# Optimization experiments

Measured on AMD Instinct MI355X. Metric: run time of the kernel, lower is better.

## Reference

```python
import jax, jax.numpy as jnp
import numpy as np

T, B, S, A, H = 512, 1024, 64, 16, 128  # timesteps, envs, state_dim, action_dim, LAYER_SIZE


def setup_inputs() -> dict:
    key = jax.random.key(0)
    ks = jax.random.split(key, 12)

    def w(k, shape, fan_in, std=1.0):
        return std * jax.random.normal(k, shape, jnp.float32) / jnp.sqrt(fan_in)

    x = jax.random.normal(ks[0], (T * B, S), jnp.float32)
    done = (jax.random.uniform(ks[1], (T * B,)) < 0.05).astype(jnp.float32)
    action = jax.random.randint(ks[2], (T * B,), 0, A, jnp.int32)
    gru_state = jnp.zeros((1, B, H), jnp.float32)

    return {
        "x": x, "done": done, "action": action, "gru_state": gru_state,
        "W1": w(ks[3], (H, S), S), "b1": jnp.zeros((H,), jnp.float32),
        "W2": w(ks[4], (H, H), H), "b2": jnp.zeros((H,), jnp.float32),
        "W_ih": w(ks[5], (3 * H, H), H), "b_ih": jnp.zeros((3 * H,), jnp.float32),
        "W_hh": w(ks[6], (3 * H, H), H), "b_hh": jnp.zeros((3 * H,), jnp.float32),
        "Wa": w(ks[7], (A, H), H, std=0.01), "ba": jnp.zeros((A,), jnp.float32),
        "Wc": w(ks[8], (1, H), H), "bc": jnp.zeros((1,), jnp.float32),
    }


def reference(x, done, action, gru_state, W1, b1, W2, b2, W_ih, b_ih, W_hh, b_hh, Wa, ba, Wc, bc):
    # MLP encoder: Linear->ReLU->Linear->ReLU  [T*B, H]
    h2 = jax.nn.relu(jax.nn.relu(x @ W1.T + b1) @ W2.T + b2)
    # Precompute input-side GRU gates for all timesteps: [T, B, 3H]
    gx = (h2 @ W_ih.T + b_ih).reshape(T, B, 3 * H)
    d = done.reshape(T, B)
    h0 = gru_state[0]  # [B, H]

    def step(h, inp):
        gx_t, d_t = inp
        h = (1.0 - d_t)[:, None] * h  # done-mask state reset
        gh = h @ W_hh.T + b_hh
        xr, xz, xn = jnp.split(gx_t, 3, axis=-1)
        hr, hz, hn = jnp.split(gh, 3, axis=-1)
        r = jax.nn.sigmoid(xr + hr)
        z = jax.nn.sigmoid(xz + hz)
        n = jnp.tanh(xn + r * hn)
        h_new = (1.0 - z) * n + z * h
        return h_new, h_new

    h_last, hs = jax.lax.scan(step, h0, (gx, d))
    hidden = hs.reshape(T * B, H)

    logits = hidden @ Wa.T + ba
    logp = jax.nn.log_softmax(logits, axis=-1)
    log_prob = jnp.take_along_axis(logp, action[:, None].astype(jnp.int32), axis=1)[:, 0]
    entropy = -jnp.sum(jnp.exp(logp) * logp, axis=-1)
    # DETACH=True: critic runs on detached hidden
    value = jax.lax.stop_gradient(hidden) @ Wc.T + bc  # [T*B, 1]

    main = jnp.concatenate([log_prob[:, None], entropy[:, None], value], axis=1)  # [T*B, 3]
    return main, h_last[None]
```

## Files before the change

kernel.cpp:

```cpp
#include <hip/hip_runtime.h>
#include <stdint.h>

#define TT 512
#define BB 1024
#define SS 64
#define HH 128
#define TBR (TT*BB)
#define NTILE (TBR/16)
#define MW_TPW 16
#define MGRID (NTILE/(4*MW_TPW))

typedef __attribute__((ext_vector_type(8))) short short8;
typedef __attribute__((ext_vector_type(4))) float floatx4;
typedef unsigned short u16;
typedef unsigned int u32;
typedef struct { u32 x, y; } u32x2;

struct TrueT  { static constexpr bool value = true;  };
struct FalseT { static constexpr bool value = false; };

__device__ __forceinline__ float bf2f(u16 u){union{u32 i;float f;}v;v.i=((u32)u)<<16;return v.f;}
__device__ __forceinline__ u16 f2bf(float f){union{float f;u32 i;}v;v.f=f;u32 r=v.i+0x7FFFu+((v.i>>16)&1u);return (u16)(r>>16);}
__device__ __forceinline__ float frcp(float x){ return __builtin_amdgcn_rcpf(x); }

__device__ __forceinline__ bool buf_is_bf16(const u16* p) {
  int ok = 0;
#pragma unroll
  for (int i = 0; i < 32; ++i) {
    u32 v = p[2*i] & 0x7FFFu;
    u32 e = v >> 7;
    ok += (v == 0u || (e >= 96u && e <= 128u)) ? 1 : 0;
  }
  return ok >= 24;
}

template<bool BF> __device__ __forceinline__ float ld1(const void* p, size_t i){
  if constexpr (BF) return bf2f(((const u16*)p)[i]);
  else              return ((const float*)p)[i];
}
__device__ __forceinline__ short8 pack8(floatx4 a, floatx4 b){
  short8 r;
  r[0]=(short)f2bf(a[0]); r[1]=(short)f2bf(a[1]); r[2]=(short)f2bf(a[2]); r[3]=(short)f2bf(a[3]);
  r[4]=(short)f2bf(b[0]); r[5]=(short)f2bf(b[1]); r[6]=(short)f2bf(b[2]); r[7]=(short)f2bf(b[3]);
  return r;
}
template<bool BF> __device__ __forceinline__ short8 ld8(const void* p, size_t i){
  if constexpr (BF) return *(const short8*)((const u16*)p + i);
  else {
    const float* f = (const float*)p + i;
    return pack8(*(const floatx4*)f, *(const floatx4*)(f + 4));
  }
}
template<bool BF> __device__ __forceinline__ void st1(void* p, size_t i, float v){
  if constexpr (BF) ((u16*)p)[i] = f2bf(v);
  else              ((float*)p)[i] = v;
}

__device__ __forceinline__ void barrier_lds() {
  __asm__ __volatile__("" ::: "memory");
  __builtin_amdgcn_s_waitcnt(0xC07F);
  __builtin_amdgcn_s_barrier();
  __asm__ __volatile__("" ::: "memory");
}

__device__ __forceinline__ int fragidx(int m,int k){
  return ((k>>5)<<9)+((m+(((k>>3)&3)<<4))<<3)+(k&7);
}
__device__ __forceinline__ floatx4 mfma(short8 a, short8 b, floatx4 c){
  return __builtin_amdgcn_mfma_f32_16x16x32_bf16(a,b,c,0,0,0);
}

template<bool BF>
__global__ __launch_bounds__(256, 2) void k_mlp(
    const void* __restrict__ x,
    const void* __restrict__ W1, const void* __restrict__ b1,
    const void* __restrict__ W2, const void* __restrict__ b2,
    u16* __restrict__ h2g)
{
  if (buf_is_bf16((const u16*)W1) != BF) return;
  const int tid = threadIdx.x, lane = tid & 63, wv = tid >> 6;
  const int n16 = lane & 15, q = lane >> 4;

  __shared__ __align__(16) u16 W2L[8*4*64*8];
  __shared__ __align__(16) u16 scr[4][2048];

  for (int s = tid; s < 2048; s += 256) {
    int j = s >> 8, ks = (s >> 6) & 3, l = s & 63;
    short8 v = ld8<BF>(W2, (size_t)(16*j + (l & 15))*HH + ks*32 + (l >> 4)*8);
    *(short8*)&W2L[(size_t)s*8] = v;
  }
  short8 w1b[8][2]; float b1v[8], b2v[8];
#pragma unroll
  for (int j = 0; j < 8; ++j) {
    int row = 16*j + n16;
#pragma unroll
    for (int ks = 0; ks < 2; ++ks) w1b[j][ks] = ld8<BF>(W1, (size_t)row*SS + ks*32 + q*8);
    b1v[j] = ld1<BF>(b1, row);
    b2v[j] = ld1<BF>(b2, row);
  }
  __syncthreads();

  u16* S = scr[wv];
  const int tile0 = (blockIdx.x * 4 + wv) * MW_TPW;

  short8 xb0, xb1; floatx4 xf0, xf1, xf2, xf3;
  {
    size_t base = ((size_t)tile0*16 + n16)*SS + q*8;
    if constexpr (BF) {
      xb0 = *(const short8*)((const u16*)x + base);
      xb1 = *(const short8*)((const u16*)x + base + 32);
    } else {
      const float* f = (const float*)x + base;
      xf0 = *(const floatx4*)f;       xf1 = *(const floatx4*)(f+4);
      xf2 = *(const floatx4*)(f+32);  xf3 = *(const floatx4*)(f+36);
    }
  }

  for (int i = 0; i < MW_TPW; ++i) {
    const int tau = tile0 + i;
    short8 xc0, xc1;
    if constexpr (BF) { xc0 = xb0; xc1 = xb1; }
    else              { xc0 = pack8(xf0, xf1); xc1 = pack8(xf2, xf3); }
    if (i + 1 < MW_TPW) {
      size_t base = ((size_t)(tau+1)*16 + n16)*SS + q*8;
      if constexpr (BF) {
        xb0 = *(const short8*)((const u16*)x + base);
        xb1 = *(const short8*)((const u16*)x + base + 32);
      } else {
        const float* f = (const float*)x + base;
        xf0 = *(const floatx4*)f;       xf1 = *(const floatx4*)(f+4);
        xf2 = *(const floatx4*)(f+32);  xf3 = *(const floatx4*)(f+36);
      }
    }
#pragma unroll
    for (int j = 0; j < 8; ++j) {
      floatx4 a = {0.f,0.f,0.f,0.f};
      a = mfma(xc0, w1b[j][0], a);
      a = mfma(xc1, w1b[j][1], a);
#pragma unroll
      for (int r = 0; r < 4; ++r) {
        float v = a[r] + b1v[j]; v = v > 0.f ? v : 0.f;
        S[fragidx(4*q + r, 16*j + n16)] = f2bf(v);
      }
    }
    short8 h1a0 = *(const short8*)(S + 0*512 + lane*8);
    short8 h1a1 = *(const short8*)(S + 1*512 + lane*8);
    short8 h1a2 = *(const short8*)(S + 2*512 + lane*8);
    short8 h1a3 = *(const short8*)(S + 3*512 + lane*8);
#pragma unroll
    for (int j = 0; j < 8; ++j) {
      floatx4 a = {0.f,0.f,0.f,0.f};
      a = mfma(h1a0, *(const short8*)&W2L[(size_t)((j*4+0)*64 + lane)*8], a);
      a = mfma(h1a1, *(const short8*)&W2L[(size_t)((j*4+1)*64 + lane)*8], a);
      a = mfma(h1a2, *(const short8*)&W2L[(size_t)((j*4+2)*64 + lane)*8], a);
      a = mfma(h1a3, *(const short8*)&W2L[(size_t)((j*4+3)*64 + lane)*8], a);
#pragma unroll
      for (int r = 0; r < 4; ++r) {
        float v = a[r] + b2v[j]; v = v > 0.f ? v : 0.f;
        S[fragidx(4*q + r, 16*j + n16)] = f2bf(v);
      }
    }
    {
      const u16* src = S + lane*32;
      u16* dst = h2g + (size_t)tau*2048 + lane*32;
      short8 d0 = *(const short8*)(src);
      short8 d1 = *(const short8*)(src + 8);
      short8 d2 = *(const short8*)(src + 16);
      short8 d3 = *(const short8*)(src + 24);
      *(short8*)(dst)      = d0;
      *(short8*)(dst + 8)  = d1;
      *(short8*)(dst + 16) = d2;
      *(short8*)(dst + 24) = d3;
    }
  }
}

template<bool BF>
__global__ __launch_bounds__(512, 2) void k_scan_split(
    const void* __restrict__ done_, const void* __restrict__ gstate,
    const void* __restrict__ Wih, const void* __restrict__ bih,
    const void* __restrict__ Whh, const void* __restrict__ bhh,
    const void* __restrict__ Wa, const void* __restrict__ ba,
    const void* __restrict__ Wc, const void* __restrict__ bc,
    const void* __restrict__ W1,
    const u16* __restrict__ h2g,
    float* __restrict__ lgws, float* __restrict__ vws,
    void* __restrict__ out)
{
  if (buf_is_bf16((const u16*)W1) != BF) return;

  const int tid = threadIdx.x, lane = tid & 63, wv = tid >> 6;
  const int n16 = lane & 15, q = lane >> 4;
  const int b0 = blockIdx.x * 16, bx = blockIdx.x;
  const int jj = 16*wv + n16;

  __shared__ __align__(16) u16 hbuf[2][2048];

  short8 wif[3][4], whf[3][4], scf[4];
  float bihv2, bhv2, bb0, bb1;
  {
    float bi0, bi1, bh0, bh1;
#pragma unroll
    for (int g = 0; g < 3; ++g) {
      int grow = g*128 + jj;
#pragma unroll
      for (int ks = 0; ks < 4; ++ks) {
        wif[g][ks] = ld8<BF>(Wih, (size_t)grow*HH + ks*32 + q*8);
        whf[g][ks] = ld8<BF>(Whh, (size_t)grow*HH + ks*32 + q*8);
      }
      float bi = ld1<BF>(bih, grow), bh = ld1<BF>(bhh, grow);
      if (g == 0) { bi0 = bi; bh0 = bh; }
      else if (g == 1) { bi1 = bi; bh1 = bh; }
      else { bihv2 = bi; bhv2 = bh; }
    }
    bb0 = bi0 + bh0;
    bb1 = bi1 + bh1;
  }
  if (wv == 1) {
#pragma unroll
    for (int ks = 0; ks < 4; ++ks) scf[ks] = ld8<BF>(Wa, (size_t)n16*HH + ks*32 + q*8);
  } else if (wv == 2) {
#pragma unroll
    for (int ks = 0; ks < 4; ++ks) {
      short8 z = {0,0,0,0,0,0,0,0};
      if (n16 == 0) z = ld8<BF>(Wc, (size_t)ks*32 + q*8);
      scf[ks] = z;
    }
  } else {
#pragma unroll
    for (int ks = 0; ks < 4; ++ks) { short8 z = {0,0,0,0,0,0,0,0}; scf[ks] = z; }
  }
  const float bav = ld1<BF>(ba, n16);
  const float bcv = ld1<BF>(bc, 0);

  float hreg[4];
#pragma unroll
  for (int r = 0; r < 4; ++r) {
    hreg[r] = ld1<BF>(gstate, (size_t)(b0 + 4*q + r)*HH + jj);
    hbuf[0][fragidx(4*q + r, jj)] = f2bf(hreg[r]);
  }
  float s4cur[2][4];
#pragma unroll
  for (int s = 0; s < 2; ++s)
#pragma unroll
    for (int r = 0; r < 4; ++r)
      s4cur[s][r] = 1.f - ld1<BF>(done_, (size_t)s*BB + b0 + 4*q + r);
  u32x2 draw[2];  floatx4 fdraw[2];
#pragma unroll
  for (int s = 0; s < 2; ++s) { draw[s].x = draw[s].y = 0; fdraw[s] = floatx4{0,0,0,0}; }

  const u16* const hz = h2g + (size_t)bx*2048;
  short8 h2p[2][4];
#pragma unroll
  for (int ks = 0; ks < 4; ++ks)
    h2p[0][ks] = *(const short8*)(hz + (size_t)0*64*2048 + ks*512 + lane*8);
#pragma unroll
  for (int ks = 0; ks < 4; ++ks)
    h2p[1][ks] = *(const short8*)(hz + (size_t)1*64*2048 + ks*512 + lane*8);
  floatx4 pipe[3];
#pragma unroll
  for (int g = 0; g < 3; ++g) {
    floatx4 a = {0.f,0.f,0.f,0.f};
#pragma unroll
    for (int ks = 0; ks < 4; ++ks) a = mfma(h2p[0][ks], wif[g][ks], a);
    pipe[g] = a;
  }
#pragma unroll
  for (int ks = 0; ks < 4; ++ks)
    h2p[0][ks] = *(const short8*)(hz + (size_t)2*64*2048 + ks*512 + lane*8);
  __syncthreads();

  u16* hw0 = &hbuf[1][0] + fragidx(4*q, jj);
  u16* hw1 = &hbuf[0][0] + fragidx(4*q, jj);

  for (int t0 = 0; t0 < TT; t0 += 2) {
#pragma unroll
    for (int s = 0; s < 2; ++s) {
      const int t = t0 + s;
      const int pw = s;
      const int pb = s ^ 1;

      short8 haf[4];
#pragma unroll
      for (int ks = 0; ks < 4; ++ks)
        haf[ks] = *(const short8*)(&hbuf[pw][0] + ks*512 + lane*8);

      floatx4 pn[3];
#pragma unroll
      for (int g = 0; g < 3; ++g) {
        floatx4 a = {0.f,0.f,0.f,0.f};
#pragma unroll
        for (int ks = 0; ks < 4; ++ks) a = mfma(h2p[pb][ks], wif[g][ks], a);
        pn[g] = a;
      }
      {
        const int tl = (t+3 < TT) ? t+3 : TT-1;
        const u16* tp = hz + (size_t)tl*64*2048;
#pragma unroll
        for (int ks = 0; ks < 4; ++ks)
          h2p[pb][ks] = *(const short8*)(tp + ks*512 + lane*8);
      }

      if (t > 0 && (wv == 1 || wv == 2)) {
        floatx4 a = {0.f,0.f,0.f,0.f};
#pragma unroll
        for (int ks = 0; ks < 4; ++ks) a = mfma(haf[ks], scf[ks], a);
        if (wv == 1) {
#pragma unroll
          for (int r = 0; r < 4; ++r)
            lgws[((size_t)(t-1)*BB + b0 + 4*q + r)*16 + n16] = a[r] + bav;
        } else if (n16 == 0) {
#pragma unroll
          for (int r = 0; r < 4; ++r)
            vws[(size_t)(t-1)*BB + b0 + 4*q + r] = a[r] + bcv;
        }
      }

      floatx4 agh[3];
#pragma unroll
      for (int g = 0; g < 3; ++g) {
        floatx4 a = {0.f,0.f,0.f,0.f};
#pragma unroll
        for (int ks = 0; ks < 4; ++ks) a = mfma(haf[ks], whf[g][ks], a);
        agh[g] = a;
      }
      u16* hw = pw ? hw1 : hw0;
#pragma unroll
      for (int r = 0; r < 4; ++r) {
        float s4 = s4cur[s][r];
        float tr = pipe[0][r] + __builtin_fmaf(s4, agh[0][r], bb0);
        float tz = pipe[1][r] + __builtin_fmaf(s4, agh[1][r], bb1);
        float xn_ = pipe[2][r] + bihv2;
        float hn_ = __builtin_fmaf(s4, agh[2][r], bhv2);
        float rg = frcp(1.f + __expf(-tr));
        float zg = frcp(1.f + __expf(-tz));
        float ni = __builtin_fmaf(rg, hn_, xn_);
        float ng = __builtin_fmaf(2.f, frcp(1.f + __expf(-2.f*ni)), -1.f);
        float hold = hreg[r] * s4;
        float hnew = __builtin_fmaf(zg, hold - ng, ng);
        hreg[r] = hnew;
        hw[r*8] = f2bf(hnew);
      }

      if (s == 0) {
#pragma unroll
        for (int ss = 0; ss < 2; ++ss) {
          const int tl = (t0+2+ss < TT) ? t0+2+ss : TT-1;
          size_t didx = (size_t)tl*BB + b0 + 4*q;
          if constexpr (BF) draw[ss] = *(const u32x2*)((const u16*)done_ + didx);
          else              fdraw[ss] = *(const floatx4*)((const float*)done_ + didx);
        }
      }

      barrier_lds();
#pragma unroll
      for (int g = 0; g < 3; ++g) pipe[g] = pn[g];
    }
    if constexpr (BF) {
#pragma unroll
      for (int ss = 0; ss < 2; ++ss) {
        s4cur[ss][0] = 1.f - bf2f((u16)(draw[ss].x & 0xFFFF));
        s4cur[ss][1] = 1.f - bf2f((u16)(draw[ss].x >> 16));
        s4cur[ss][2] = 1.f - bf2f((u16)(draw[ss].y & 0xFFFF));
        s4cur[ss][3] = 1.f - bf2f((u16)(draw[ss].y >> 16));
      }
    } else {
#pragma unroll
      for (int ss = 0; ss < 2; ++ss)
#pragma unroll
        for (int r = 0; r < 4; ++r) s4cur[ss][r] = 1.f - fdraw[ss][r];
    }
  }

  {
    if (wv == 1 || wv == 2) {
      short8 haf[4];
#pragma unroll
      for (int ks = 0; ks < 4; ++ks) haf[ks] = *(const short8*)(&hbuf[0][0] + ks*512 + lane*8);
      floatx4 a = {0.f,0.f,0.f,0.f};
#pragma unroll
      for (int ks = 0; ks < 4; ++ks) a = mfma(haf[ks], scf[ks], a);
      if (wv == 1) {
#pragma unroll
        for (int r = 0; r < 4; ++r)
          lgws[((size_t)(TT-1)*BB + b0 + 4*q + r)*16 + n16] = a[r] + bav;
      } else if (n16 == 0) {
#pragma unroll
        for (int r = 0; r < 4; ++r)
          vws[(size_t)(TT-1)*BB + b0 + 4*q + r] = a[r] + bcv;
      }
    }
#pragma unroll
    for (int r = 0; r < 4; ++r)
      st1<BF>(out, (size_t)3*TBR + (size_t)(b0 + 4*q + r)*HH + jj, hreg[r]);
  }
}

template<bool BF>
__global__ __launch_bounds__(512, 2) void k_scan_mono(
    const void* __restrict__ x, const void* __restrict__ done_,
    const void* __restrict__ gstate,
    const void* __restrict__ W1, const void* __restrict__ b1,
    const void* __restrict__ W2, const void* __restrict__ b2,
    const void* __restrict__ Wih, const void* __restrict__ bih,
    const void* __restrict__ Whh, const void* __restrict__ bhh,
    const void* __restrict__ Wa, const void* __restrict__ ba,
    const void* __restrict__ Wc, const void* __restrict__ bc,
    float* __restrict__ lgws, float* __restrict__ vws,
    void* __restrict__ out)
{
  if (buf_is_bf16((const u16*)W1) != BF) return;

  const int tid = threadIdx.x, lane = tid & 63, wv = tid >> 6;
  const int n16 = lane & 15, q = lane >> 4;
  const int b0 = blockIdx.x * 16;
  const int jj = 16*wv + n16;

  __shared__ __align__(16) u16 hbuf[2][2048];
  __shared__ __align__(16) u16 h1f[2][2048];
  __shared__ __align__(16) u16 h2f[2][2048];

  short8 w1f[2], w2f[4], wif[3][4], whf[3][4], scf[4];
  float b1v, b2v, bihv2, bhv2, bb0, bb1;
  {
    int row = wv*16 + n16;
#pragma unroll
    for (int ks = 0; ks < 2; ++ks) w1f[ks] = ld8<BF>(W1, (size_t)row*SS + ks*32 + q*8);
    b1v = ld1<BF>(b1, row);
#pragma unroll
    for (int ks = 0; ks < 4; ++ks) w2f[ks] = ld8<BF>(W2, (size_t)row*HH + ks*32 + q*8);
    b2v = ld1<BF>(b2, row);
    float bi0, bi1, bh0, bh1;
#pragma unroll
    for (int g = 0; g < 3; ++g) {
      int grow = g*128 + jj;
#pragma unroll
      for (int ks = 0; ks < 4; ++ks) {
        wif[g][ks] = ld8<BF>(Wih, (size_t)grow*HH + ks*32 + q*8);
        whf[g][ks] = ld8<BF>(Whh, (size_t)grow*HH + ks*32 + q*8);
      }
      float bi = ld1<BF>(bih, grow), bh = ld1<BF>(bhh, grow);
      if (g == 0) { bi0 = bi; bh0 = bh; }
      else if (g == 1) { bi1 = bi; bh1 = bh; }
      else { bihv2 = bi; bhv2 = bh; }
    }
    bb0 = bi0 + bh0;
    bb1 = bi1 + bh1;
  }
  if (wv == 1) {
#pragma unroll
    for (int ks = 0; ks < 4; ++ks) scf[ks] = ld8<BF>(Wa, (size_t)n16*HH + ks*32 + q*8);
  } else if (wv == 2) {
#pragma unroll
    for (int ks = 0; ks < 4; ++ks) {
      short8 z = {0,0,0,0,0,0,0,0};
      if (n16 == 0) z = ld8<BF>(Wc, (size_t)ks*32 + q*8);
      scf[ks] = z;
    }
  } else {
#pragma unroll
    for (int ks = 0; ks < 4; ++ks) { short8 z = {0,0,0,0,0,0,0,0}; scf[ks] = z; }
  }
  const float bav = ld1<BF>(ba, n16);
  const float bcv = ld1<BF>(bc, 0);

  float hreg[4];
#pragma unroll
  for (int r = 0; r < 4; ++r) {
    hreg[r] = ld1<BF>(gstate, (size_t)(b0 + 4*q + r)*HH + jj);
    hbuf[0][fragidx(4*q + r, jj)] = f2bf(hreg[r]);
  }
  short8 xc[2][2], xn[2][2];
#pragma unroll
  for (int s = 0; s < 2; ++s)
#pragma unroll
    for (int ks = 0; ks < 2; ++ks)
      xc[s][ks] = ld8<BF>(x, ((size_t)s*BB + b0 + n16)*SS + ks*32 + q*8);
  float s4cur[2][4];
#pragma unroll
  for (int s = 0; s < 2; ++s)
#pragma unroll
    for (int r = 0; r < 4; ++r) s4cur[s][r] = 1.f;
  u32x2 draw[2];  floatx4 fdraw[2];
#pragma unroll
  for (int s = 0; s < 2; ++s) { draw[s].x = draw[s].y = 0; fdraw[s] = floatx4{0,0,0,0}; }
#pragma unroll
  for (int s = 0; s < 2; ++s)
#pragma unroll
    for (int ks = 0; ks < 2; ++ks) { short8 z={0,0,0,0,0,0,0,0}; xn[s][ks]=z; }
  floatx4 pipe[2][3];
#pragma unroll
  for (int s = 0; s < 2; ++s)
#pragma unroll
    for (int g = 0; g < 3; ++g) pipe[s][g] = floatx4{0.f,0.f,0.f,0.f};
  __syncthreads();

  u16* hw0 = &hbuf[1][0] + fragidx(4*q, jj);
  u16* hw1 = &hbuf[0][0] + fragidx(4*q, jj);

  auto iter = [&](int t0, auto steady) {
    constexpr bool ST = decltype(steady)::value;
#pragma unroll
    for (int s = 0; s < 2; ++s) {
      const int t = t0 + s;
      const bool s1on = ST || (t <= TT-5);
      const bool s2on = ST || (t >= -3 && t <= TT-4);
      const bool s3on = ST || (t >= -2 && t <= TT-3);
      const bool ron  = ST || (t >= 0);
      const int pw = t & 1;

      short8 haf[4];
      if (ron) {
#pragma unroll
        for (int ks = 0; ks < 4; ++ks)
          haf[ks] = *(const short8*)(&hbuf[pw][0] + ks*512 + lane*8);
      }
      if (s1on) {
        floatx4 a = {0.f,0.f,0.f,0.f};
        a = mfma(xc[s][0], w1f[0], a);
        a = mfma(xc[s][1], w1f[1], a);
#pragma unroll
        for (int r = 0; r < 4; ++r) {
          float v = a[r] + b1v; v = v > 0.f ? v : 0.f;
          h1f[pw][fragidx(4*q + r, jj)] = f2bf(v);
        }
      }
      if (s2on) {
        short8 h1a[4];
#pragma unroll
        for (int ks = 0; ks < 4; ++ks)
          h1a[ks] = *(const short8*)(&h1f[pw^1][0] + ks*512 + lane*8);
        floatx4 a = {0.f,0.f,0.f,0.f};
#pragma unroll
        for (int ks = 0; ks < 4; ++ks) a = mfma(h1a[ks], w2f[ks], a);
#pragma unroll
        for (int r = 0; r < 4; ++r) {
          float v = a[r] + b2v; v = v > 0.f ? v : 0.f;
          h2f[pw][fragidx(4*q + r, jj)] = f2bf(v);
        }
      }
      if (s == 0) {
        if (ST || (t0 + 6 < TT)) {
          if constexpr (BF) {
#pragma unroll
            for (int ss = 0; ss < 2; ++ss) {
              size_t base = ((size_t)(t0+6+ss)*BB + b0 + n16)*SS + q*8;
              xn[ss][0] = *(const short8*)((const u16*)x + base);
              xn[ss][1] = *(const short8*)((const u16*)x + base + 32);
            }
          }
        }
        if (ST || (t0+2 >= 0 && t0+2 < TT)) {
#pragma unroll
          for (int ss = 0; ss < 2; ++ss) {
            size_t didx = (size_t)(t0+2+ss)*BB + b0 + 4*q;
            if constexpr (BF) draw[ss] = *(const u32x2*)((const u16*)done_ + didx);
            else              fdraw[ss] = *(const floatx4*)((const float*)done_ + didx);
          }
        }
      }
      if (ron) {
        if (t > 0 && (wv == 1 || wv == 2)) {
          floatx4 a = {0.f,0.f,0.f,0.f};
#pragma unroll
          for (int ks = 0; ks < 4; ++ks) a = mfma(haf[ks], scf[ks], a);
          if (wv == 1) {
#pragma unroll
            for (int r = 0; r < 4; ++r)
              lgws[((size_t)(t-1)*BB + b0 + 4*q + r)*16 + n16] = a[r] + bav;
          } else if (n16 == 0) {
#pragma unroll
            for (int r = 0; r < 4; ++r)
              vws[(size_t)(t-1)*BB + b0 + 4*q + r] = a[r] + bcv;
          }
        }
        floatx4 agh[3];
#pragma unroll
        for (int g = 0; g < 3; ++g) {
          floatx4 a = {0.f,0.f,0.f,0.f};
#pragma unroll
          for (int ks = 0; ks < 4; ++ks) a = mfma(haf[ks], whf[g][ks], a);
          agh[g] = a;
        }
        u16* hw = pw ? hw1 : hw0;
#pragma unroll
        for (int r = 0; r < 4; ++r) {
          float s4 = s4cur[s][r];
          float tr = pipe[s][0][r] + __builtin_fmaf(s4, agh[0][r], bb0);
          float tz = pipe[s][1][r] + __builtin_fmaf(s4, agh[1][r], bb1);
          float xn_ = pipe[s][2][r] + bihv2;
          float hn_ = __builtin_fmaf(s4, agh[2][r], bhv2);
          float rg = frcp(1.f + __expf(-tr));
          float zg = frcp(1.f + __expf(-tz));
          float ni = __builtin_fmaf(rg, hn_, xn_);
          float ng = __builtin_fmaf(2.f, frcp(1.f + __expf(-2.f*ni)), -1.f);
          float hold = hreg[r] * s4;
          float hnew = __builtin_fmaf(zg, hold - ng, ng);
          hreg[r] = hnew;
          hw[r*8] = f2bf(hnew);
        }
      }
      if (s3on) {
        short8 h2a[4];
#pragma unroll
        for (int ks = 0; ks < 4; ++ks)
          h2a[ks] = *(const short8*)(&h2f[pw^1][0] + ks*512 + lane*8);
#pragma unroll
        for (int g = 0; g < 3; ++g) {
          floatx4 a = {0.f,0.f,0.f,0.f};
#pragma unroll
          for (int ks = 0; ks < 4; ++ks) a = mfma(h2a[ks], wif[g][ks], a);
          pipe[s][g] = a;
        }
      }
      barrier_lds();
    }
    if (ST || (t0 + 6 < TT)) {
      if constexpr (BF) {
#pragma unroll
        for (int ss = 0; ss < 2; ++ss) { xc[ss][0] = xn[ss][0]; xc[ss][1] = xn[ss][1]; }
      } else {
#pragma unroll
        for (int ss = 0; ss < 2; ++ss) {
          size_t base = ((size_t)(t0+6+ss)*BB + b0 + n16)*SS + q*8;
          xc[ss][0] = ld8<false>(x, base);
          xc[ss][1] = ld8<false>(x, base + 32);
        }
      }
    }
    if (ST || (t0+2 >= 0 && t0+2 < TT)) {
      if constexpr (BF) {
#pragma unroll
        for (int ss = 0; ss < 2; ++ss) {
          s4cur[ss][0] = 1.f - bf2f((u16)(draw[ss].x & 0xFFFF));
          s4cur[ss][1] = 1.f - bf2f((u16)(draw[ss].x >> 16));
          s4cur[ss][2] = 1.f - bf2f((u16)(draw[ss].y & 0xFFFF));
          s4cur[ss][3] = 1.f - bf2f((u16)(draw[ss].y >> 16));
        }
      } else {
#pragma unroll
        for (int ss = 0; ss < 2; ++ss)
#pragma unroll
          for (int r = 0; r < 4; ++r) s4cur[ss][r] = 1.f - fdraw[ss][r];
      }
    }
  };

  iter(-4, FalseT{});
  iter(-2, FalseT{});
  for (int t0 = 0; t0 <= TT - 8; t0 += 2) iter(t0, TrueT{});
  iter(TT-6, FalseT{});
  iter(TT-4, FalseT{});
  iter(TT-2, FalseT{});

  {
    if (wv == 1 || wv == 2) {
      short8 haf[4];
#pragma unroll
      for (int ks = 0; ks < 4; ++ks) haf[ks] = *(const short8*)(&hbuf[0][0] + ks*512 + lane*8);
      floatx4 a = {0.f,0.f,0.f,0.f};
#pragma unroll
      for (int ks = 0; ks < 4; ++ks) a = mfma(haf[ks], scf[ks], a);
      if (wv == 1) {
#pragma unroll
        for (int r = 0; r < 4; ++r)
          lgws[((size_t)(TT-1)*BB + b0 + 4*q + r)*16 + n16] = a[r] + bav;
      } else if (n16 == 0) {
#pragma unroll
        for (int r = 0; r < 4; ++r)
          vws[(size_t)(TT-1)*BB + b0 + 4*q + r] = a[r] + bcv;
      }
    }
#pragma unroll
    for (int r = 0; r < 4; ++r)
      st1<BF>(out, (size_t)3*TBR + (size_t)(b0 + 4*q + r)*HH + jj, hreg[r]);
  }
}

template<bool BF>
__global__ __launch_bounds__(256) void k_head(
    const float* __restrict__ lgws, const float* __restrict__ vws,
    const int* __restrict__ action, const void* __restrict__ W1,
    void* __restrict__ out)
{
  if (buf_is_bf16((const u16*)W1) != BF) return;
  size_t row = (size_t)blockIdx.x * 256 + threadIdx.x;
  if (row >= (size_t)TBR) return;
  const float* lp = lgws + row*16;
  floatx4 v[4];
#pragma unroll
  for (int i = 0; i < 4; ++i) v[i] = *(const floatx4*)(lp + 4*i);
  float mx = v[0][0];
#pragma unroll
  for (int i = 0; i < 4; ++i)
#pragma unroll
    for (int j = 0; j < 4; ++j) mx = fmaxf(mx, v[i][j]);
  float sum = 0.f, se = 0.f;
#pragma unroll
  for (int i = 0; i < 4; ++i)
#pragma unroll
    for (int j = 0; j < 4; ++j) {
      float d = v[i][j] - mx;
      float e = __expf(d);
      sum += e; se = __builtin_fmaf(e, d, se);
    }
  float ls = __logf(sum);
  int a = action[row];
  float la = lp[a];
  float lpa = (la - mx) - ls;
  float ent = ls - se * frcp(sum);
  st1<BF>(out, row*3,     lpa);
  st1<BF>(out, row*3 + 1, ent);
  st1<BF>(out, row*3 + 2, vws[row]);
}

extern "C" void kernel_launch(void* const* d_in, const int* in_sizes, int n_in,
                              void* d_out, int out_size, void* d_ws, size_t ws_size,
                              hipStream_t stream) {
  const void* x    = d_in[0];
  const void* done = d_in[1];
  const int*  act  = (const int*)d_in[2];
  const void* gst  = d_in[3];
  const void* W1   = d_in[4];
  const void* b1   = d_in[5];
  const void* W2   = d_in[6];
  const void* b2   = d_in[7];
  const void* Wih  = d_in[8];
  const void* bih  = d_in[9];
  const void* Whh  = d_in[10];
  const void* bhh  = d_in[11];
  const void* Wa   = d_in[12];
  const void* ba   = d_in[13];
  const void* Wc   = d_in[14];
  const void* bc   = d_in[15];

  float* lgws = (float*)d_ws;
  float* vws  = lgws + (size_t)16*TBR;
  u16*   h2g  = (u16*)(vws + (size_t)TBR);
  const size_t need = (size_t)(16*TBR + TBR)*4 + (size_t)NTILE*4096;

  if (ws_size >= need) {
    hipLaunchKernelGGL((k_mlp<true>),  dim3(MGRID), dim3(256), 0, stream,
                       x, W1, b1, W2, b2, h2g);
    hipLaunchKernelGGL((k_mlp<false>), dim3(MGRID), dim3(256), 0, stream,
                       x, W1, b1, W2, b2, h2g);
    hipLaunchKernelGGL((k_scan_split<true>),  dim3(64), dim3(512), 0, stream,
                       done, gst, Wih, bih, Whh, bhh, Wa, ba, Wc, bc,
                       W1, h2g, lgws, vws, d_out);
    hipLaunchKernelGGL((k_scan_split<false>), dim3(64), dim3(512), 0, stream,
                       done, gst, Wih, bih, Whh, bhh, Wa, ba, Wc, bc,
                       W1, h2g, lgws, vws, d_out);
  } else {
    hipLaunchKernelGGL((k_scan_mono<true>),  dim3(64), dim3(512), 0, stream,
                       x, done, gst, W1, b1, W2, b2, Wih, bih,
                       Whh, bhh, Wa, ba, Wc, bc, lgws, vws, d_out);
    hipLaunchKernelGGL((k_scan_mono<false>), dim3(64), dim3(512), 0, stream,
                       x, done, gst, W1, b1, W2, b2, Wih, bih,
                       Whh, bhh, Wa, ba, Wc, bc, lgws, vws, d_out);
  }
  hipLaunchKernelGGL((k_head<true>),  dim3(TBR/256), dim3(256), 0, stream,
                     lgws, vws, act, W1, d_out);
  hipLaunchKernelGGL((k_head<false>), dim3(TBR/256), dim3(256), 0, stream,
                     lgws, vws, act, W1, d_out);
}
```

Baseline: 758.9 us.

## Merge dtype-templated kernel pairs into single runtime-dispatch kernels and restructure MLP

Replaces each pair of bf16/fp32 templated launches with one kernel that checks the dtype at runtime, which removes three launches and the no-op blocks they started. The MLP kernel moves from 256-thread blocks with W2 staged in LDS to 64-thread single-wave blocks that keep W2 in registers, and loads x directly each iteration on the fp32 path instead of prefetching it. The scan kernel starts its input-gate accumulators at the folded bias so the per-step bias additions go away, and it rotates the pipeline buffers by swapping arguments instead of copying. The trade-off is higher register pressure in the MLP (128 more VGPRs for W2) and both dtype paths compiled into every kernel.

```diff
diff --git a/kernel.cpp b/kernel.cpp
--- a/kernel.cpp
+++ b/kernel.cpp
@@ -8,7 +8,7 @@
 #define TBR (TT*BB)
 #define NTILE (TBR/16)
 #define MW_TPW 16
-#define MGRID (NTILE/(4*MW_TPW))
+#define MGRID (NTILE/MW_TPW)
 
 typedef __attribute__((ext_vector_type(8))) short short8;
 typedef __attribute__((ext_vector_type(4))) float floatx4;
@@ -16,9 +16,6 @@
 typedef unsigned int u32;
 typedef struct { u32 x, y; } u32x2;
 
-struct TrueT  { static constexpr bool value = true;  };
-struct FalseT { static constexpr bool value = false; };
-
 __device__ __forceinline__ float bf2f(u16 u){union{u32 i;float f;}v;v.i=((u32)u)<<16;return v.f;}
 __device__ __forceinline__ u16 f2bf(float f){union{float f;u32 i;}v;v.f=f;u32 r=v.i+0x7FFFu+((v.i>>16)&1u);return (u16)(r>>16);}
 __device__ __forceinline__ float frcp(float x){ return __builtin_amdgcn_rcpf(x); }
@@ -71,66 +68,51 @@
 }
 
 template<bool BF>
-__global__ __launch_bounds__(256, 2) void k_mlp(
+__device__ __forceinline__ void mlp_u_body(
     const void* __restrict__ x,
     const void* __restrict__ W1, const void* __restrict__ b1,
     const void* __restrict__ W2, const void* __restrict__ b2,
-    u16* __restrict__ h2g)
+    u16* __restrict__ h2g, u16* S)
 {
-  if (buf_is_bf16((const u16*)W1) != BF) return;
-  const int tid = threadIdx.x, lane = tid & 63, wv = tid >> 6;
+  const int lane = threadIdx.x & 63;
   const int n16 = lane & 15, q = lane >> 4;
 
-  __shared__ __align__(16) u16 W2L[8*4*64*8];
-  __shared__ __align__(16) u16 scr[4][2048];
-
-  for (int s = tid; s < 2048; s += 256) {
-    int j = s >> 8, ks = (s >> 6) & 3, l = s & 63;
-    short8 v = ld8<BF>(W2, (size_t)(16*j + (l & 15))*HH + ks*32 + (l >> 4)*8);
-    *(short8*)&W2L[(size_t)s*8] = v;
-  }
-  short8 w1b[8][2]; float b1v[8], b2v[8];
+  short8 w1b[8][2], w2b[8][4];
+  float b1v[8], b2v[8];
 #pragma unroll
   for (int j = 0; j < 8; ++j) {
     int row = 16*j + n16;
 #pragma unroll
     for (int ks = 0; ks < 2; ++ks) w1b[j][ks] = ld8<BF>(W1, (size_t)row*SS + ks*32 + q*8);
+#pragma unroll
+    for (int ks = 0; ks < 4; ++ks) w2b[j][ks] = ld8<BF>(W2, (size_t)row*HH + ks*32 + q*8);
     b1v[j] = ld1<BF>(b1, row);
     b2v[j] = ld1<BF>(b2, row);
   }
-  __syncthreads();
-
-  u16* S = scr[wv];
-  const int tile0 = (blockIdx.x * 4 + wv) * MW_TPW;
-
-  short8 xb0, xb1; floatx4 xf0, xf1, xf2, xf3;
-  {
+
+  const int tile0 = blockIdx.x * MW_TPW;
+
+  short8 xb0, xb1;
+  if constexpr (BF) {
     size_t base = ((size_t)tile0*16 + n16)*SS + q*8;
-    if constexpr (BF) {
-      xb0 = *(const short8*)((const u16*)x + base);
-      xb1 = *(const short8*)((const u16*)x + base + 32);
-    } else {
-      const float* f = (const float*)x + base;
-      xf0 = *(const floatx4*)f;       xf1 = *(const floatx4*)(f+4);
-      xf2 = *(const floatx4*)(f+32);  xf3 = *(const floatx4*)(f+36);
-    }
+    xb0 = *(const short8*)((const u16*)x + base);
+    xb1 = *(const short8*)((const u16*)x + base + 32);
   }
 
   for (int i = 0; i < MW_TPW; ++i) {
     const int tau = tile0 + i;
     short8 xc0, xc1;
-    if constexpr (BF) { xc0 = xb0; xc1 = xb1; }
-    else              { xc0 = pack8(xf0, xf1); xc1 = pack8(xf2, xf3); }
-    if (i + 1 < MW_TPW) {
-      size_t base = ((size_t)(tau+1)*16 + n16)*SS + q*8;
-      if constexpr (BF) {
+    if constexpr (BF) {
+      xc0 = xb0; xc1 = xb1;
+      if (i + 1 < MW_TPW) {
+        size_t base = ((size_t)(tau+1)*16 + n16)*SS + q*8;
         xb0 = *(const short8*)((const u16*)x + base);
         xb1 = *(const short8*)((const u16*)x + base + 32);
-      } else {
-        const float* f = (const float*)x + base;
-        xf0 = *(const floatx4*)f;       xf1 = *(const floatx4*)(f+4);
-        xf2 = *(const floatx4*)(f+32);  xf3 = *(const floatx4*)(f+36);
-      }
+      }
+    } else {
+      const float* f = (const float*)x + ((size_t)tau*16 + n16)*SS + q*8;
+      xc0 = pack8(*(const floatx4*)f, *(const floatx4*)(f+4));
+      xc1 = pack8(*(const floatx4*)(f+32), *(const floatx4*)(f+36));
     }
 #pragma unroll
     for (int j = 0; j < 8; ++j) {
@@ -150,10 +132,10 @@
 #pragma unroll
     for (int j = 0; j < 8; ++j) {
       floatx4 a = {0.f,0.f,0.f,0.f};
-      a = mfma(h1a0, *(const short8*)&W2L[(size_t)((j*4+0)*64 + lane)*8], a);
-      a = mfma(h1a1, *(const short8*)&W2L[(size_t)((j*4+1)*64 + lane)*8], a);
-      a = mfma(h1a2, *(const short8*)&W2L[(size_t)((j*4+2)*64 + lane)*8], a);
-      a = mfma(h1a3, *(const short8*)&W2L[(size_t)((j*4+3)*64 + lane)*8], a);
+      a = mfma(h1a0, w2b[j][0], a);
+      a = mfma(h1a1, w2b[j][1], a);
+      a = mfma(h1a2, w2b[j][2], a);
+      a = mfma(h1a3, w2b[j][3], a);
 #pragma unroll
       for (int r = 0; r < 4; ++r) {
         float v = a[r] + b2v[j]; v = v > 0.f ? v : 0.f;
@@ -175,8 +157,233 @@
   }
 }
 
+__global__ __launch_bounds__(64, 2) void k_mlp_u(
+    const void* __restrict__ x,
+    const void* __restrict__ W1, const void* __restrict__ b1,
+    const void* __restrict__ W2, const void* __restrict__ b2,
+    u16* __restrict__ h2g)
+{
+  __shared__ __align__(16) u16 S[2048];
+  if (buf_is_bf16((const u16*)W1)) mlp_u_body<true >(x, W1, b1, W2, b2, h2g, S);
+  else                             mlp_u_body<false>(x, W1, b1, W2, b2, h2g, S);
+}
+
 template<bool BF>
-__global__ __launch_bounds__(512, 2) void k_scan_split(
+__device__ __forceinline__ void scan_body(
+    const void* __restrict__ done_, const void* __restrict__ gstate,
+    const void* __restrict__ Wih, const void* __restrict__ bih,
+    const void* __restrict__ Whh, const void* __restrict__ bhh,
+    const void* __restrict__ Wa, const void* __restrict__ ba,
+    const void* __restrict__ Wc, const void* __restrict__ bc,
+    const u16* __restrict__ h2g,
+    float* __restrict__ lgws, float* __restrict__ vws,
+    void* __restrict__ out, int bx, u16 (*hbuf)[2048])
+{
+  const int tid = threadIdx.x, lane = tid & 63, wv = tid >> 6;
+  const int n16 = lane & 15, q = lane >> 4;
+  const int b0 = bx * 16;
+  const int jj = 16*wv + n16;
+
+  short8 wif[3][4], whf[3][4], scf[4];
+  float bihv2, bhv2, bb0, bb1;
+  {
+    float bi0, bi1, bh0, bh1;
+#pragma unroll
+    for (int g = 0; g < 3; ++g) {
+      int grow = g*128 + jj;
+#pragma unroll
+      for (int ks = 0; ks < 4; ++ks) {
+        wif[g][ks] = ld8<BF>(Wih, (size_t)grow*HH + ks*32 + q*8);
+        whf[g][ks] = ld8<BF>(Whh, (size_t)grow*HH + ks*32 + q*8);
+      }
+      float bi = ld1<BF>(bih, grow), bh = ld1<BF>(bhh, grow);
+      if (g == 0) { bi0 = bi; bh0 = bh; }
+      else if (g == 1) { bi1 = bi; bh1 = bh; }
+      else { bihv2 = bi; bhv2 = bh; }
+    }
+    bb0 = bi0 + bh0;
+    bb1 = bi1 + bh1;
+  }
+  if (wv == 1) {
+#pragma unroll
+    for (int ks = 0; ks < 4; ++ks) scf[ks] = ld8<BF>(Wa, (size_t)n16*HH + ks*32 + q*8);
+  } else if (wv == 2) {
+#pragma unroll
+    for (int ks = 0; ks < 4; ++ks) {
+      short8 z = {0,0,0,0,0,0,0,0};
+      if (n16 == 0) z = ld8<BF>(Wc, (size_t)ks*32 + q*8);
+      scf[ks] = z;
+    }
+  } else {
+#pragma unroll
+    for (int ks = 0; ks < 4; ++ks) { short8 z = {0,0,0,0,0,0,0,0}; scf[ks] = z; }
+  }
+  const float bav = ld1<BF>(ba, n16);
+  const float bcv = ld1<BF>(bc, 0);
+  const float ginit[3] = {bb0, bb1, bihv2};
+
+  float hreg[4];
+#pragma unroll
+  for (int r = 0; r < 4; ++r) {
+    hreg[r] = ld1<BF>(gstate, (size_t)(b0 + 4*q + r)*HH + jj);
+    hbuf[0][fragidx(4*q + r, jj)] = f2bf(hreg[r]);
+  }
+  float s4cur[2][4];
+#pragma unroll
+  for (int s = 0; s < 2; ++s)
+#pragma unroll
+    for (int r = 0; r < 4; ++r)
+      s4cur[s][r] = 1.f - ld1<BF>(done_, (size_t)s*BB + b0 + 4*q + r);
+  u32x2 draw[2];  floatx4 fdraw[2];
+#pragma unroll
+  for (int s = 0; s < 2; ++s) { draw[s].x = draw[s].y = 0; fdraw[s] = floatx4{0,0,0,0}; }
+
+  const u16* const hz = h2g + (size_t)bx*2048;
+  short8 h2p0[4], h2p1[4];
+#pragma unroll
+  for (int ks = 0; ks < 4; ++ks)
+    h2p0[ks] = *(const short8*)(hz + (size_t)0*64*2048 + ks*512 + lane*8);
+#pragma unroll
+  for (int ks = 0; ks < 4; ++ks)
+    h2p1[ks] = *(const short8*)(hz + (size_t)1*64*2048 + ks*512 + lane*8);
+  floatx4 pipeA[3], pipeB[3];
+#pragma unroll
+  for (int g = 0; g < 3; ++g) {
+    float gv = ginit[g];
+    floatx4 a = {gv, gv, gv, gv};
+#pragma unroll
+    for (int ks = 0; ks < 4; ++ks) a = mfma(h2p0[ks], wif[g][ks], a);
+    pipeA[g] = a;
+  }
+#pragma unroll
+  for (int ks = 0; ks < 4; ++ks)
+    h2p0[ks] = *(const short8*)(hz + (size_t)2*64*2048 + ks*512 + lane*8);
+  __syncthreads();
+
+  u16* hw0 = &hbuf[1][0] + fragidx(4*q, jj);
+  u16* hw1 = &hbuf[0][0] + fragidx(4*q, jj);
+
+  auto step = [&](int t, const u16* hb_rd, u16* hw, floatx4 (&pin)[3],
+                  floatx4 (&pout)[3], short8 (&hp)[4], float (&s4r)[4],
+                  bool dopf) {
+    short8 haf[4];
+#pragma unroll
+    for (int ks = 0; ks < 4; ++ks)
+      haf[ks] = *(const short8*)(hb_rd + ks*512 + lane*8);
+
+#pragma unroll
+    for (int g = 0; g < 3; ++g) {
+      float gv = ginit[g];
+      floatx4 a = {gv, gv, gv, gv};
+#pragma unroll
+      for (int ks = 0; ks < 4; ++ks) a = mfma(hp[ks], wif[g][ks], a);
+      pout[g] = a;
+    }
+    {
+      const int tl = (t+3 < TT) ? t+3 : TT-1;
+      const u16* tp = hz + (size_t)tl*64*2048;
+#pragma unroll
+      for (int ks = 0; ks < 4; ++ks)
+        hp[ks] = *(const short8*)(tp + ks*512 + lane*8);
+    }
+
+    if (t > 0 && (wv == 1 || wv == 2)) {
+      floatx4 a = {0.f,0.f,0.f,0.f};
+#pragma unroll
+      for (int ks = 0; ks < 4; ++ks) a = mfma(haf[ks], scf[ks], a);
+      if (wv == 1) {
+#pragma unroll
+        for (int r = 0; r < 4; ++r)
+          lgws[((size_t)(t-1)*BB + b0 + 4*q + r)*16 + n16] = a[r] + bav;
+      } else if (n16 == 0) {
+#pragma unroll
+        for (int r = 0; r < 4; ++r)
+          vws[(size_t)(t-1)*BB + b0 + 4*q + r] = a[r] + bcv;
+      }
+    }
+
+    floatx4 agh[3];
+#pragma unroll
+    for (int g = 0; g < 3; ++g) {
+      floatx4 a = {0.f,0.f,0.f,0.f};
+#pragma unroll
+      for (int ks = 0; ks < 4; ++ks) a = mfma(haf[ks], whf[g][ks], a);
+      agh[g] = a;
+    }
+#pragma unroll
+    for (int r = 0; r < 4; ++r) {
+      float s4 = s4r[r];
+      float tr = __builtin_fmaf(s4, agh[0][r], pin[0][r]);
+      float tz = __builtin_fmaf(s4, agh[1][r], pin[1][r]);
+      float xn_ = pin[2][r];
+      float hn_ = __builtin_fmaf(s4, agh[2][r], bhv2);
+      float rg = frcp(1.f + __expf(-tr));
+      float zg = frcp(1.f + __expf(-tz));
+      float ni = __builtin_fmaf(rg, hn_, xn_);
+      float ng = __builtin_fmaf(2.f, frcp(1.f + __expf(-2.f*ni)), -1.f);
+      float hold = hreg[r] * s4;
+      float hnew = __builtin_fmaf(zg, hold - ng, ng);
+      hreg[r] = hnew;
+      hw[r*8] = f2bf(hnew);
+    }
+
+    if (dopf) {
+#pragma unroll
+      for (int ss = 0; ss < 2; ++ss) {
+        const int tl = (t+2+ss < TT) ? t+2+ss : TT-1;
+        size_t didx = (size_t)tl*BB + b0 + 4*q;
+        if constexpr (BF) draw[ss] = *(const u32x2*)((const u16*)done_ + didx);
+        else              fdraw[ss] = *(const floatx4*)((const float*)done_ + didx);
+      }
+    }
+
+    barrier_lds();
+  };
+
+  for (int t0 = 0; t0 < TT; t0 += 2) {
+    step(t0,     &hbuf[0][0], hw0, pipeA, pipeB, h2p1, s4cur[0], true);
+    step(t0 + 1, &hbuf[1][0], hw1, pipeB, pipeA, h2p0, s4cur[1], false);
+    if constexpr (BF) {
+#pragma unroll
+      for (int ss = 0; ss < 2; ++ss) {
+        s4cur[ss][0] = 1.f - bf2f((u16)(draw[ss].x & 0xFFFF));
+        s4cur[ss][1] = 1.f - bf2f((u16)(draw[ss].x >> 16));
+        s4cur[ss][2] = 1.f - bf2f((u16)(draw[ss].y & 0xFFFF));
+        s4cur[ss][3] = 1.f - bf2f((u16)(draw[ss].y >> 16));
+      }
+    } else {
+#pragma unroll
+      for (int ss = 0; ss < 2; ++ss)
+#pragma unroll
+        for (int r = 0; r < 4; ++r) s4cur[ss][r] = 1.f - fdraw[ss][r];
+    }
+  }
+
+  {
+    if (wv == 1 || wv == 2) {
+      short8 haf[4];
+#pragma unroll
+      for (int ks = 0; ks < 4; ++ks) haf[ks] = *(const short8*)(&hbuf[0][0] + ks*512 + lane*8);
+      floatx4 a = {0.f,0.f,0.f,0.f};
+#pragma unroll
+      for (int ks = 0; ks < 4; ++ks) a = mfma(haf[ks], scf[ks], a);
+      if (wv == 1) {
+#pragma unroll
+        for (int r = 0; r < 4; ++r)
+          lgws[((size_t)(TT-1)*BB + b0 + 4*q + r)*16 + n16] = a[r] + bav;
+      } else if (n16 == 0) {
+#pragma unroll
+        for (int r = 0; r < 4; ++r)
+          vws[(size_t)(TT-1)*BB + b0 + 4*q + r] = a[r] + bcv;
+      }
+    }
+#pragma unroll
+    for (int r = 0; r < 4; ++r)
+      st1<BF>(out, (size_t)3*TBR + (size_t)(b0 + 4*q + r)*HH + jj, hreg[r]);
+  }
+}
+
+__global__ __launch_bounds__(512, 2) void k_scan_u(
     const void* __restrict__ done_, const void* __restrict__ gstate,
     const void* __restrict__ Wih, const void* __restrict__ bih,
     const void* __restrict__ Whh, const void* __restrict__ bhh,
@@ -187,214 +394,17 @@
     float* __restrict__ lgws, float* __restrict__ vws,
     void* __restrict__ out)
 {
-  if (buf_is_bf16((const u16*)W1) != BF) return;
-
-  const int tid = threadIdx.x, lane = tid & 63, wv = tid >> 6;
-  const int n16 = lane & 15, q = lane >> 4;
-  const int b0 = blockIdx.x * 16, bx = blockIdx.x;
-  const int jj = 16*wv + n16;
-
   __shared__ __align__(16) u16 hbuf[2][2048];
-
-  short8 wif[3][4], whf[3][4], scf[4];
-  float bihv2, bhv2, bb0, bb1;
-  {
-    float bi0, bi1, bh0, bh1;
-#pragma unroll
-    for (int g = 0; g < 3; ++g) {
-      int grow = g*128 + jj;
-#pragma unroll
-      for (int ks = 0; ks < 4; ++ks) {
-        wif[g][ks] = ld8<BF>(Wih, (size_t)grow*HH + ks*32 + q*8);
-        whf[g][ks] = ld8<BF>(Whh, (size_t)grow*HH + ks*32 + q*8);
-      }
-      float bi = ld1<BF>(bih, grow), bh = ld1<BF>(bhh, grow);
-      if (g == 0) { bi0 = bi; bh0 = bh; }
-      else if (g == 1) { bi1 = bi; bh1 = bh; }
-      else { bihv2 = bi; bhv2 = bh; }
-    }
-    bb0 = bi0 + bh0;
-    bb1 = bi1 + bh1;
-  }
-  if (wv == 1) {
-#pragma unroll
-    for (int ks = 0; ks < 4; ++ks) scf[ks] = ld8<BF>(Wa, (size_t)n16*HH + ks*32 + q*8);
-  } else if (wv == 2) {
-#pragma unroll
-    for (int ks = 0; ks < 4; ++ks) {
-      short8 z = {0,0,0,0,0,0,0,0};
-      if (n16 == 0) z = ld8<BF>(Wc, (size_t)ks*32 + q*8);
-      scf[ks] = z;
-    }
-  } else {
-#pragma unroll
-    for (int ks = 0; ks < 4; ++ks) { short8 z = {0,0,0,0,0,0,0,0}; scf[ks] = z; }
-  }
-  const float bav = ld1<BF>(ba, n16);
-  const float bcv = ld1<BF>(bc, 0);
-
-  float hreg[4];
-#pragma unroll
-  for (int r = 0; r < 4; ++r) {
-    hreg[r] = ld1<BF>(gstate, (size_t)(b0 + 4*q + r)*HH + jj);
-    hbuf[0][fragidx(4*q + r, jj)] = f2bf(hreg[r]);
-  }
-  float s4cur[2][4];
-#pragma unroll
-  for (int s = 0; s < 2; ++s)
-#pragma unroll
-    for (int r = 0; r < 4; ++r)
-      s4cur[s][r] = 1.f - ld1<BF>(done_, (size_t)s*BB + b0 + 4*q + r);
-  u32x2 draw[2];  floatx4 fdraw[2];
-#pragma unroll
-  for (int s = 0; s < 2; ++s) { draw[s].x = draw[s].y = 0; fdraw[s] = floatx4{0,0,0,0}; }
-
-  const u16* const hz = h2g + (size_t)bx*2048;
-  short8 h2p[2][4];
-#pragma unroll
-  for (int ks = 0; ks < 4; ++ks)
-    h2p[0][ks] = *(const short8*)(hz + (size_t)0*64*2048 + ks*512 + lane*8);
-#pragma unroll
-  for (int ks = 0; ks < 4; ++ks)
-    h2p[1][ks] = *(const short8*)(hz + (size_t)1*64*2048 + ks*512 + lane*8);
-  floatx4 pipe[3];
-#pragma unroll
-  for (int g = 0; g < 3; ++g) {
-    floatx4 a = {0.f,0.f,0.f,0.f};
-#pragma unroll
-    for (int ks = 0; ks < 4; ++ks) a = mfma(h2p[0][ks], wif[g][ks], a);
-    pipe[g] = a;
-  }
-#pragma unroll
-  for (int ks = 0; ks < 4; ++ks)
-    h2p[0][ks] = *(const short8*)(hz + (size_t)2*64*2048 + ks*512 + lane*8);
-  __syncthreads();
-
-  u16* hw0 = &hbuf[1][0] + fragidx(4*q, jj);
-  u16* hw1 = &hbuf[0][0] + fragidx(4*q, jj);
-
-  for (int t0 = 0; t0 < TT; t0 += 2) {
-#pragma unroll
-    for (int s = 0; s < 2; ++s) {
-      const int t = t0 + s;
-      const int pw = s;
-      const int pb = s ^ 1;
-
-      short8 haf[4];
-#pragma unroll
-      for (int ks = 0; ks < 4; ++ks)
-        haf[ks] = *(const short8*)(&hbuf[pw][0] + ks*512 + lane*8);
-
-      floatx4 pn[3];
-#pragma unroll
-      for (int g = 0; g < 3; ++g) {
-        floatx4 a = {0.f,0.f,0.f,0.f};
-#pragma unroll
-        for (int ks = 0; ks < 4; ++ks) a = mfma(h2p[pb][ks], wif[g][ks], a);
-        pn[g] = a;
-      }
-      {
-        const int tl = (t+3 < TT) ? t+3 : TT-1;
-        const u16* tp = hz + (size_t)tl*64*2048;
-#pragma unroll
-        for (int ks = 0; ks < 4; ++ks)
-          h2p[pb][ks] = *(const short8*)(tp + ks*512 + lane*8);
-      }
-
-      if (t > 0 && (wv == 1 || wv == 2)) {
-        floatx4 a = {0.f,0.f,0.f,0.f};
-#pragma unroll
-        for (int ks = 0; ks < 4; ++ks) a = mfma(haf[ks], scf[ks], a);
-        if (wv == 1) {
-#pragma unroll
-          for (int r = 0; r < 4; ++r)
-            lgws[((size_t)(t-1)*BB + b0 + 4*q + r)*16 + n16] = a[r] + bav;
-        } else if (n16 == 0) {
-#pragma unroll
-          for (int r = 0; r < 4; ++r)
-            vws[(size_t)(t-1)*BB + b0 + 4*q + r] = a[r] + bcv;
-        }
-      }
-
-      floatx4 agh[3];
-#pragma unroll
-      for (int g = 0; g < 3; ++g) {
-        floatx4 a = {0.f,0.f,0.f,0.f};
-#pragma unroll
-        for (int ks = 0; ks < 4; ++ks) a = mfma(haf[ks], whf[g][ks], a);
-        agh[g] = a;
-      }
-      u16* hw = pw ? hw1 : hw0;
-#pragma unroll
-      for (int r = 0; r < 4; ++r) {
-        float s4 = s4cur[s][r];
-        float tr = pipe[0][r] + __builtin_fmaf(s4, agh[0][r], bb0);
-        float tz = pipe[1][r] + __builtin_fmaf(s4, agh[1][r], bb1);
-        float xn_ = pipe[2][r] + bihv2;
-        float hn_ = __builtin_fmaf(s4, agh[2][r], bhv2);
-        float rg = frcp(1.f + __expf(-tr));
-        float zg = frcp(1.f + __expf(-tz));
-        float ni = __builtin_fmaf(rg, hn_, xn_);
-        float ng = __builtin_fmaf(2.f, frcp(1.f + __expf(-2.f*ni)), -1.f);
-        float hold = hreg[r] * s4;
-        float hnew = __builtin_fmaf(zg, hold - ng, ng);
-        hreg[r] = hnew;
-        hw[r*8] = f2bf(hnew);
-      }
-
-      if (s == 0) {
-#pragma unroll
-        for (int ss = 0; ss < 2; ++ss) {
-          const int tl = (t0+2+ss < TT) ? t0+2+ss : TT-1;
-          size_t didx = (size_t)tl*BB + b0 + 4*q;
-          if constexpr (BF) draw[ss] = *(const u32x2*)((const u16*)done_ + didx);
-          else              fdraw[ss] = *(const floatx4*)((const float*)done_ + didx);
-        }
-      }
-
-      barrier_lds();
-#pragma unroll
-      for (int g = 0; g < 3; ++g) pipe[g] = pn[g];
-    }
-    if constexpr (BF) {
-#pragma unroll
-      for (int ss = 0; ss < 2; ++ss) {
-        s4cur[ss][0] = 1.f - bf2f((u16)(draw[ss].x & 0xFFFF));
-        s4cur[ss][1] = 1.f - bf2f((u16)(draw[ss].x >> 16));
-        s4cur[ss][2] = 1.f - bf2f((u16)(draw[ss].y & 0xFFFF));
-        s4cur[ss][3] = 1.f - bf2f((u16)(draw[ss].y >> 16));
-      }
-    } else {
-#pragma unroll
-      for (int ss = 0; ss < 2; ++ss)
-#pragma unroll
-        for (int r = 0; r < 4; ++r) s4cur[ss][r] = 1.f - fdraw[ss][r];
-    }
-  }
-
-  {
-    if (wv == 1 || wv == 2) {
-      short8 haf[4];
-#pragma unroll
-      for (int ks = 0; ks < 4; ++ks) haf[ks] = *(const short8*)(&hbuf[0][0] + ks*512 + lane*8);
-      floatx4 a = {0.f,0.f,0.f,0.f};
-#pragma unroll
-      for (int ks = 0; ks < 4; ++ks) a = mfma(haf[ks], scf[ks], a);
-      if (wv == 1) {
-#pragma unroll
-        for (int r = 0; r < 4; ++r)
-          lgws[((size_t)(TT-1)*BB + b0 + 4*q + r)*16 + n16] = a[r] + bav;
-      } else if (n16 == 0) {
-#pragma unroll
-        for (int r = 0; r < 4; ++r)
-          vws[(size_t)(TT-1)*BB + b0 + 4*q + r] = a[r] + bcv;
-      }
-    }
-#pragma unroll
-    for (int r = 0; r < 4; ++r)
-      st1<BF>(out, (size_t)3*TBR + (size_t)(b0 + 4*q + r)*HH + jj, hreg[r]);
-  }
-}
+  if (buf_is_bf16((const u16*)W1))
+    scan_body<true >(done_, gstate, Wih, bih, Whh, bhh, Wa, ba, Wc, bc,
+                     h2g, lgws, vws, out, blockIdx.x, hbuf);
+  else
+    scan_body<false>(done_, gstate, Wih, bih, Whh, bhh, Wa, ba, Wc, bc,
+                     h2g, lgws, vws, out, blockIdx.x, hbuf);
+}
+
+struct TrueT  { static constexpr bool value = true;  };
+struct FalseT { static constexpr bool value = false; };
 
 template<bool BF>
 __global__ __launch_bounds__(512, 2) void k_scan_mono(
@@ -677,13 +687,12 @@
   }
 }
 
-template<bool BF>
-__global__ __launch_bounds__(256) void k_head(
+__global__ __launch_bounds__(256) void k_head_u(
     const float* __restrict__ lgws, const float* __restrict__ vws,
     const int* __restrict__ action, const void* __restrict__ W1,
     void* __restrict__ out)
 {
-  if (buf_is_bf16((const u16*)W1) != BF) return;
+  const bool bf = buf_is_bf16((const u16*)W1);
   size_t row = (size_t)blockIdx.x * 256 + threadIdx.x;
   if (row >= (size_t)TBR) return;
   const float* lp = lgws + row*16;
@@ -709,9 +718,16 @@
   float la = lp[a];
   float lpa = (la - mx) - ls;
   float ent = ls - se * frcp(sum);
-  st1<BF>(out, row*3,     lpa);
-  st1<BF>(out, row*3 + 1, ent);
-  st1<BF>(out, row*3 + 2, vws[row]);
+  float val = vws[row];
+  if (bf) {
+    st1<true>(out, row*3,     lpa);
+    st1<true>(out, row*3 + 1, ent);
+    st1<true>(out, row*3 + 2, val);
+  } else {
+    st1<false>(out, row*3,     lpa);
+    st1<false>(out, row*3 + 1, ent);
+    st1<false>(out, row*3 + 2, val);
+  }
 }
 
 extern "C" void kernel_launch(void* const* d_in, const int* in_sizes, int n_in,
@@ -740,14 +756,9 @@
   const size_t need = (size_t)(16*TBR + TBR)*4 + (size_t)NTILE*4096;
 
   if (ws_size >= need) {
-    hipLaunchKernelGGL((k_mlp<true>),  dim3(MGRID), dim3(256), 0, stream,
+    hipLaunchKernelGGL(k_mlp_u, dim3(MGRID), dim3(64), 0, stream,
                        x, W1, b1, W2, b2, h2g);
-    hipLaunchKernelGGL((k_mlp<false>), dim3(MGRID), dim3(256), 0, stream,
-                       x, W1, b1, W2, b2, h2g);
-    hipLaunchKernelGGL((k_scan_split<true>),  dim3(64), dim3(512), 0, stream,
-                       done, gst, Wih, bih, Whh, bhh, Wa, ba, Wc, bc,
-                       W1, h2g, lgws, vws, d_out);
-    hipLaunchKernelGGL((k_scan_split<false>), dim3(64), dim3(512), 0, stream,
+    hipLaunchKernelGGL(k_scan_u, dim3(64), dim3(512), 0, stream,
                        done, gst, Wih, bih, Whh, bhh, Wa, ba, Wc, bc,
                        W1, h2g, lgws, vws, d_out);
   } else {
@@ -758,8 +769,6 @@
                        x, done, gst, W1, b1, W2, b2, Wih, bih,
                        Whh, bhh, Wa, ba, Wc, bc, lgws, vws, d_out);
   }
-  hipLaunchKernelGGL((k_head<true>),  dim3(TBR/256), dim3(256), 0, stream,
+  hipLaunchKernelGGL(k_head_u, dim3(TBR/256), dim3(256), 0, stream,
                      lgws, vws, act, W1, d_out);
-  hipLaunchKernelGGL((k_head<false>), dim3(TBR/256), dim3(256), 0, stream,
-                     lgws, vws, act, W1, d_out);
-}
+}
```

Measured after the change: 762.2 us. Within noise of the previous version (+0.4%).
